# Kernel optimization log

Measured on AMD Instinct MI355X. Metric: run time of the kernel, lower is better.

## Reference

```python
import math
import jax, jax.numpy as jnp
from jax import lax
import numpy as np

SPARSITY = 0.05
EMBEDDING_SIZE = 2048
BATCH = 32768


def setup_inputs() -> dict:
    key = jax.random.key(0)
    k0, k1, k2 = jax.random.split(key, 3)
    x = jax.random.normal(k0, (BATCH, 28, 28), dtype=jnp.float32)
    # conv: out=5, in=1, k=3, no bias (kaiming-ish scale)
    conv_w = jax.random.normal(k1, (5, 1, 3, 3), dtype=jnp.float32) * (1.0 / math.sqrt(9))
    bn_gamma = jnp.ones((5,), jnp.float32)
    bn_beta = jnp.zeros((5,), jnp.float32)
    bn_mean = jnp.zeros((5,), jnp.float32)
    bn_var = jnp.ones((5,), jnp.float32)
    # fc: [EMBEDDING_SIZE, 320], no bias
    fc_w = jax.random.normal(k2, (EMBEDDING_SIZE, 5 * 8 * 8), dtype=jnp.float32) * (1.0 / math.sqrt(320))
    return {"x": x, "conv_w": conv_w, "bn_gamma": bn_gamma, "bn_beta": bn_beta,
            "bn_mean": bn_mean, "bn_var": bn_var, "fc_w": fc_w}


def _kwta(z):
    # k-winners-take-all: top k_active entries per row -> 1, rest -> 0.
    k_active = math.ceil(SPARSITY * z.shape[1])
    topv, _ = lax.top_k(z, k_active)          # [B, k]
    thr = topv[:, -1:]                         # kth largest per row
    binary = (z >= thr).astype(z.dtype)
    # straight-through: forward = binary, backward = identity
    return z + lax.stop_gradient(binary - z)


def reference(x, conv_w, bn_gamma, bn_beta, bn_mean, bn_var, fc_w):
    h = x[:, None, :, :]  # [B,1,28,28]
    h = lax.conv_general_dilated(h, conv_w, window_strides=(1, 1), padding="VALID",
                                 dimension_numbers=("NCHW", "OIHW", "NCHW"))  # [B,5,26,26]
    inv_std = bn_gamma / jnp.sqrt(bn_var + 1e-5)
    h = (h - bn_mean[None, :, None, None]) * inv_std[None, :, None, None] + bn_beta[None, :, None, None]
    h = jnp.maximum(h, 0.0)
    # max_pool2d(kernel=3, stride=3), floor mode -> [B,5,8,8]
    h = lax.reduce_window(h, -jnp.inf, lax.max, (1, 1, 3, 3), (1, 1, 3, 3), "VALID")
    h = h.reshape(h.shape[0], -1)              # [B,320]
    z = h @ fc_w.T                             # [B,EMBEDDING_SIZE]
    return _kwta(z)
```

## Files before the change

kernel.cpp:

```cpp
#include <hip/hip_runtime.h>
#include <math.h>

#define BATCH 32768
#define EMB   2048
#define KDIM  320
#define KACT  103

#define BM 16
#define GTHREADS 1024

#define CIMG 16

#define HSTRIDE 260

__global__ __launch_bounds__(256) void transpose_w_kernel(const float* __restrict__ W,
                                                          float* __restrict__ WT) {
  __shared__ float tile[32][33];
  const int k0 = blockIdx.x * 32;
  const int n0 = blockIdx.y * 32;
  const int tx = threadIdx.x;
  const int ty = threadIdx.y;
  for (int i = ty; i < 32; i += 8)
    tile[i][tx] = W[(size_t)(n0 + i) * KDIM + k0 + tx];
  __syncthreads();
  for (int i = ty; i < 32; i += 8)
    WT[(size_t)(k0 + i) * EMB + n0 + tx] = tile[tx][i];
}

__global__ __launch_bounds__(512) void conv_pool_kernel(const float* __restrict__ x,
                                                        const float* __restrict__ cw,
                                                        const float* __restrict__ gamma,
                                                        const float* __restrict__ beta,
                                                        const float* __restrict__ mean,
                                                        const float* __restrict__ var,
                                                        float* __restrict__ Ht) {
#pragma clang fp contract(off)
  __shared__ float xs[CIMG * 784];
  __shared__ float hs[KDIM * 17];
  __shared__ float wv[45];
  __shared__ float inv_s[5], mu_s[5], be_s[5];
  const int t  = threadIdx.x;
  const int b0 = blockIdx.x * CIMG;

  {
    const float4* src = (const float4*)(x + (size_t)b0 * 784);
    float4* dst = (float4*)xs;
    for (int i = t; i < CIMG * 196; i += 512) dst[i] = src[i];
  }
  if (t < 45) wv[t] = cw[t];
  if (t < 5) {
    inv_s[t] = gamma[t] / sqrtf(var[t] + 1e-5f);
    mu_s[t] = mean[t];
    be_s[t] = beta[t];
  }
  __syncthreads();

  const int i0   = t >> 6;
  const int lane = t & 63;
  const int py = lane >> 3;
  const int px = lane & 7;

  for (int ii = 0; ii < 2; ++ii) {
    const int img = i0 * 2 + ii;
    const float* xb = xs + img * 784;

    float xr[5][5];
#pragma unroll
    for (int i = 0; i < 5; ++i)
#pragma unroll
      for (int j = 0; j < 5; ++j)
        xr[i][j] = xb[(3 * py + i) * 28 + 3 * px + j];

#pragma unroll
    for (int c = 0; c < 5; ++c) {
      float wr[9];
#pragma unroll
      for (int i = 0; i < 9; ++i) wr[i] = wv[c * 9 + i];
      const float inv = inv_s[c], mu = mu_s[c], be = be_s[c];
      float mx = -__builtin_huge_valf();
#pragma unroll
      for (int ry = 0; ry < 3; ++ry)
#pragma unroll
        for (int rx = 0; rx < 3; ++rx) {
          float s = 0.0f;
#pragma unroll
          for (int di = 0; di < 3; ++di)
#pragma unroll
            for (int dj = 0; dj < 3; ++dj)
              s = __builtin_fmaf(xr[ry + di][rx + dj], wr[di * 3 + dj], s);
          float t1 = s - mu;
          float t2 = t1 * inv;
          float t3 = t2 + be;
          mx = fmaxf(mx, t3);
        }
      hs[(c * 64 + lane) * 17 + img] = fmaxf(mx, 0.0f);
    }
  }
  __syncthreads();

  float* dst = Ht + (size_t)blockIdx.x * (KDIM * CIMG);
  for (int i = t; i < KDIM * CIMG; i += 512) {
    const int k = i >> 4;
    const int img = i & 15;
    dst[i] = hs[k * 17 + img];
  }
}

__global__ __launch_bounds__(GTHREADS, 8) void gemm_topk_kernel(const float* __restrict__ Ht,
                                                                const float* __restrict__ WT,
                                                                float* __restrict__ out) {
  __shared__ unsigned histo[BM * HSTRIDE];
  __shared__ unsigned prefix_s[BM];
  __shared__ unsigned rank_s[BM];

  const int t    = threadIdx.x;
  const int lane = t & 63;
  const int w    = t >> 6;
  const int m0   = blockIdx.x * BM;
  const int nt   = t * 2;

  if (t < BM) { prefix_s[t] = 0u; rank_s[t] = KACT; }

  float acc[BM][2];
#pragma unroll
  for (int m = 0; m < BM; ++m) {
    acc[m][0] = 0.0f;
    acc[m][1] = 0.0f;
  }

  const float* Ap = Ht + (size_t)blockIdx.x * (KDIM * BM);
  const float* wp = WT + nt;

#pragma unroll 4
  for (int k = 0; k < KDIM; ++k) {
    const float* ak = Ap + (size_t)k * BM;
    float av[BM];
#pragma unroll
    for (int m = 0; m < BM; ++m) av[m] = ak[m];
    const float2 bb = *(const float2*)(wp + (size_t)k * EMB);
#pragma unroll
    for (int m = 0; m < BM; ++m) {
      acc[m][0] = __builtin_fmaf(av[m], bb.x, acc[m][0]);
      acc[m][1] = __builtin_fmaf(av[m], bb.y, acc[m][1]);
    }
  }
  __syncthreads();

  for (int pass = 0; pass < 4; ++pass) {
    const int shift = 24 - pass * 8;
    for (int i = t; i < BM * HSTRIDE; i += GTHREADS) histo[i] = 0u;
    unsigned pref[BM];
#pragma unroll
    for (int m = 0; m < BM; ++m) pref[m] = prefix_s[m];
    __syncthreads();
#pragma unroll
    for (int m = 0; m < BM; ++m) {
#pragma unroll
      for (int j = 0; j < 2; ++j) {
        unsigned u = __float_as_uint(acc[m][j]);
        u = (u & 0x80000000u) ? ~u : (u | 0x80000000u);
        const bool in = (pass == 0) || ((u >> (shift + 8)) == pref[m]);
        if (in) atomicAdd(&histo[m * HSTRIDE + ((u >> shift) & 255u)], 1u);
      }
    }
    __syncthreads();
    {
      const int m = w;
      const unsigned rank = rank_s[m];
      const uint4 c = *(const uint4*)(histo + m * HSTRIDE + lane * 4);
      const unsigned s = c.x + c.y + c.z + c.w;
      unsigned suf = s;
#pragma unroll
      for (int off = 1; off < 64; off <<= 1) {
        const unsigned o = __shfl_down(suf, off);
        if (lane + off < 64) suf += o;
      }
      const unsigned above = suf - s;
      if (above < rank && rank <= suf) {
        unsigned bin, newr;
        if (above + c.w >= rank)                    { bin = lane * 4 + 3; newr = rank - above; }
        else if (above + c.w + c.z >= rank)         { bin = lane * 4 + 2; newr = rank - above - c.w; }
        else if (above + c.w + c.z + c.y >= rank)   { bin = lane * 4 + 1; newr = rank - above - c.w - c.z; }
        else                                        { bin = lane * 4 + 0; newr = rank - above - c.w - c.z - c.y; }
        prefix_s[m] = (prefix_s[m] << 8) | bin;
        rank_s[m] = newr;
      }
    }
    __syncthreads();
  }

  unsigned thr[BM];
#pragma unroll
  for (int m = 0; m < BM; ++m) thr[m] = prefix_s[m];

#pragma unroll
  for (int m = 0; m < BM; ++m) {
    float2 o;
#pragma unroll
    for (int j = 0; j < 2; ++j) {
      unsigned u = __float_as_uint(acc[m][j]);
      u = (u & 0x80000000u) ? ~u : (u | 0x80000000u);
      ((float*)&o)[j] = (u >= thr[m]) ? 1.0f : 0.0f;
    }
    *(float2*)(out + (size_t)(m0 + m) * EMB + nt) = o;
  }
}

extern "C" void kernel_launch(void* const* d_in, const int* in_sizes, int n_in,
                              void* d_out, int out_size, void* d_ws, size_t ws_size,
                              hipStream_t stream) {
  const float* x      = (const float*)d_in[0];
  const float* conv_w = (const float*)d_in[1];
  const float* gamma  = (const float*)d_in[2];
  const float* beta   = (const float*)d_in[3];
  const float* mean   = (const float*)d_in[4];
  const float* var    = (const float*)d_in[5];
  const float* fc_w   = (const float*)d_in[6];
  float* out = (float*)d_out;

  float* Ht = (float*)d_ws;
  float* WT = (float*)d_ws + (size_t)KDIM * BATCH;

  transpose_w_kernel<<<dim3(KDIM / 32, EMB / 32), dim3(32, 8), 0, stream>>>(fc_w, WT);
  conv_pool_kernel<<<BATCH / CIMG, 512, 0, stream>>>(x, conv_w, gamma, beta, mean, var, Ht);
  gemm_topk_kernel<<<BATCH / BM, GTHREADS, 0, stream>>>(Ht, WT, out);
}
```

Before: 833.0 us.

## Replace shared-memory radix histogram top-k with per-wave ballot bitwise threshold search

Swaps the 4-pass 8-bit radix histogram selection, which relies on shared atomics, for a bit-by-bit binary search of the k-th largest key. Each wave loads one row of 2048 values from LDS into registers and counts candidates with ballot/popcount across 32 bit iterations. Rows are staged through an 8-row LDS buffer in two halves, so the block's 16 waves each take one row. This removes atomic contention and the histogram clears, but it adds 32 serial iterations of 32 ballots per wave and extra barriers.

```diff
diff --git a/kernel.cpp b/kernel.cpp
--- a/kernel.cpp
+++ b/kernel.cpp
@@ -10,8 +10,6 @@
 #define GTHREADS 1024
 
 #define CIMG 16
-
-#define HSTRIDE 260
 
 __global__ __launch_bounds__(256) void transpose_w_kernel(const float* __restrict__ W,
                                                           float* __restrict__ WT) {
@@ -109,9 +107,8 @@
 __global__ __launch_bounds__(GTHREADS, 8) void gemm_topk_kernel(const float* __restrict__ Ht,
                                                                 const float* __restrict__ WT,
                                                                 float* __restrict__ out) {
-  __shared__ unsigned histo[BM * HSTRIDE];
-  __shared__ unsigned prefix_s[BM];
-  __shared__ unsigned rank_s[BM];
+  __shared__ float zb[8][EMB];
+  __shared__ unsigned thr_s[BM];
 
   const int t    = threadIdx.x;
   const int lane = t & 63;
@@ -119,8 +116,6 @@
   const int m0   = blockIdx.x * BM;
   const int nt   = t * 2;
 
-  if (t < BM) { prefix_s[t] = 0u; rank_s[t] = KACT; }
-
   float acc[BM][2];
 #pragma unroll
   for (int m = 0; m < BM; ++m) {
@@ -144,64 +139,81 @@
       acc[m][1] = __builtin_fmaf(av[m], bb.y, acc[m][1]);
     }
   }
-  __syncthreads();
-
-  for (int pass = 0; pass < 4; ++pass) {
-    const int shift = 24 - pass * 8;
-    for (int i = t; i < BM * HSTRIDE; i += GTHREADS) histo[i] = 0u;
-    unsigned pref[BM];
-#pragma unroll
-    for (int m = 0; m < BM; ++m) pref[m] = prefix_s[m];
-    __syncthreads();
-#pragma unroll
-    for (int m = 0; m < BM; ++m) {
-#pragma unroll
-      for (int j = 0; j < 2; ++j) {
-        unsigned u = __float_as_uint(acc[m][j]);
-        u = (u & 0x80000000u) ? ~u : (u | 0x80000000u);
-        const bool in = (pass == 0) || ((u >> (shift + 8)) == pref[m]);
-        if (in) atomicAdd(&histo[m * HSTRIDE + ((u >> shift) & 255u)], 1u);
-      }
-    }
-    __syncthreads();
-    {
-      const int m = w;
-      const unsigned rank = rank_s[m];
-      const uint4 c = *(const uint4*)(histo + m * HSTRIDE + lane * 4);
-      const unsigned s = c.x + c.y + c.z + c.w;
-      unsigned suf = s;
-#pragma unroll
-      for (int off = 1; off < 64; off <<= 1) {
-        const unsigned o = __shfl_down(suf, off);
-        if (lane + off < 64) suf += o;
-      }
-      const unsigned above = suf - s;
-      if (above < rank && rank <= suf) {
-        unsigned bin, newr;
-        if (above + c.w >= rank)                    { bin = lane * 4 + 3; newr = rank - above; }
-        else if (above + c.w + c.z >= rank)         { bin = lane * 4 + 2; newr = rank - above - c.w; }
-        else if (above + c.w + c.z + c.y >= rank)   { bin = lane * 4 + 1; newr = rank - above - c.w - c.z; }
-        else                                        { bin = lane * 4 + 0; newr = rank - above - c.w - c.z - c.y; }
-        prefix_s[m] = (prefix_s[m] << 8) | bin;
-        rank_s[m] = newr;
-      }
-    }
-    __syncthreads();
-  }
-
-  unsigned thr[BM];
-#pragma unroll
-  for (int m = 0; m < BM; ++m) thr[m] = prefix_s[m];
-
-#pragma unroll
-  for (int m = 0; m < BM; ++m) {
+
+#pragma unroll
+  for (int m = 0; m < 8; ++m)
+    *(float2*)&zb[m][nt] = *(const float2*)&acc[8 + m][0];
+  __syncthreads();
+
+  if (w >= 8) {
+    const unsigned* row = (const unsigned*)&zb[w - 8][0];
+    unsigned v[32];
+#pragma unroll
+    for (int j = 0; j < 32; ++j) {
+      const unsigned x = row[j * 64 + lane];
+      v[j] = x ^ (unsigned)(((int)x >> 31) | 0x80000000);
+    }
+    unsigned T = 0u;
+    for (int b = 31; b >= 0; --b) {
+      const unsigned cand = T | (1u << b);
+      unsigned cnt = 0u;
+#pragma unroll
+      for (int j = 0; j < 32; ++j)
+        cnt += (unsigned)__popcll(__ballot(v[j] >= cand));
+      if (cnt >= KACT) T = cand;
+    }
+    if (lane == 0) thr_s[w] = T;
+  }
+  __syncthreads();
+
+#pragma unroll
+  for (int m = 0; m < 8; ++m) {
+    const float2 p = *(const float2*)&zb[m][nt];
+    const unsigned thr = thr_s[8 + m];
+    unsigned ux = __float_as_uint(p.x); ux ^= (unsigned)(((int)ux >> 31) | 0x80000000);
+    unsigned uy = __float_as_uint(p.y); uy ^= (unsigned)(((int)uy >> 31) | 0x80000000);
     float2 o;
-#pragma unroll
-    for (int j = 0; j < 2; ++j) {
-      unsigned u = __float_as_uint(acc[m][j]);
-      u = (u & 0x80000000u) ? ~u : (u | 0x80000000u);
-      ((float*)&o)[j] = (u >= thr[m]) ? 1.0f : 0.0f;
-    }
+    o.x = (ux >= thr) ? 1.0f : 0.0f;
+    o.y = (uy >= thr) ? 1.0f : 0.0f;
+    *(float2*)(out + (size_t)(m0 + 8 + m) * EMB + nt) = o;
+  }
+  __syncthreads();
+
+#pragma unroll
+  for (int m = 0; m < 8; ++m)
+    *(float2*)&zb[m][nt] = *(const float2*)&acc[m][0];
+  __syncthreads();
+
+  if (w < 8) {
+    const unsigned* row = (const unsigned*)&zb[w][0];
+    unsigned v[32];
+#pragma unroll
+    for (int j = 0; j < 32; ++j) {
+      const unsigned x = row[j * 64 + lane];
+      v[j] = x ^ (unsigned)(((int)x >> 31) | 0x80000000);
+    }
+    unsigned T = 0u;
+    for (int b = 31; b >= 0; --b) {
+      const unsigned cand = T | (1u << b);
+      unsigned cnt = 0u;
+#pragma unroll
+      for (int j = 0; j < 32; ++j)
+        cnt += (unsigned)__popcll(__ballot(v[j] >= cand));
+      if (cnt >= KACT) T = cand;
+    }
+    if (lane == 0) thr_s[w] = T;
+  }
+  __syncthreads();
+
+#pragma unroll
+  for (int m = 0; m < 8; ++m) {
+    const float2 p = *(const float2*)&zb[m][nt];
+    const unsigned thr = thr_s[m];
+    unsigned ux = __float_as_uint(p.x); ux ^= (unsigned)(((int)ux >> 31) | 0x80000000);
+    unsigned uy = __float_as_uint(p.y); uy ^= (unsigned)(((int)uy >> 31) | 0x80000000);
+    float2 o;
+    o.x = (ux >= thr) ? 1.0f : 0.0f;
+    o.y = (uy >= thr) ? 1.0f : 0.0f;
     *(float2*)(out + (size_t)(m0 + m) * EMB + nt) = o;
   }
 }
```

Result: slower. 884.8 us (+6.2%).

## Fuse conv/pool stage into the GEMM+top-k kernel in one launch

Applied to the files above, without the earlier changes.

Merges the conv+BN+ReLU+pool kernel into the GEMM/top-k kernel, so each 1024-thread block computes features for its 16 images and then does the GEMM and radix-select top-k. Shared memory is aliased so the input tile, feature buffer and histogram share one array. Features are still written to global memory and read back through a separate pointer, relying on block-local visibility after __syncthreads. This removes one launch and lets conv work overlap other blocks' GEMM, at the cost of larger shared memory per block and possibly lower occupancy.

```diff
diff --git a/kernel.cpp b/kernel.cpp
--- a/kernel.cpp
+++ b/kernel.cpp
@@ -8,7 +8,6 @@
 
 #define BM 16
 #define GTHREADS 1024
-
 #define CIMG 16
 
 #define HSTRIDE 260
@@ -27,25 +26,37 @@
     WT[(size_t)(k0 + i) * EMB + n0 + tx] = tile[tx][i];
 }
 
-__global__ __launch_bounds__(512) void conv_pool_kernel(const float* __restrict__ x,
-                                                        const float* __restrict__ cw,
-                                                        const float* __restrict__ gamma,
-                                                        const float* __restrict__ beta,
-                                                        const float* __restrict__ mean,
-                                                        const float* __restrict__ var,
-                                                        float* __restrict__ Ht) {
+__global__ __launch_bounds__(GTHREADS, 8) void fused_conv_gemm_topk(
+    const float* __restrict__ x,
+    const float* __restrict__ cw,
+    const float* __restrict__ gamma,
+    const float* __restrict__ beta,
+    const float* __restrict__ mean,
+    const float* __restrict__ var,
+    float* __restrict__ HtW,
+    const float* __restrict__ HtR,
+    const float* __restrict__ WT,
+    float* __restrict__ out) {
 #pragma clang fp contract(off)
-  __shared__ float xs[CIMG * 784];
-  __shared__ float hs[KDIM * 17];
+  __shared__ __attribute__((aligned(16))) float smem[17984];
   __shared__ float wv[45];
   __shared__ float inv_s[5], mu_s[5], be_s[5];
-  const int t  = threadIdx.x;
-  const int b0 = blockIdx.x * CIMG;
+  __shared__ unsigned prefix_s[BM];
+  __shared__ unsigned rank_s[BM];
+
+  float* const xs = smem;
+  float* const hs = smem + 12544;
+  unsigned* const histo = (unsigned*)smem;
+
+  const int t    = threadIdx.x;
+  const int lane = t & 63;
+  const int w    = t >> 6;
+  const int b0   = blockIdx.x * CIMG;
 
   {
     const float4* src = (const float4*)(x + (size_t)b0 * 784);
     float4* dst = (float4*)xs;
-    for (int i = t; i < CIMG * 196; i += 512) dst[i] = src[i];
+    for (int i = t; i < CIMG * 196; i += GTHREADS) dst[i] = src[i];
   }
   if (t < 45) wv[t] = cw[t];
   if (t < 5) {
@@ -55,14 +66,11 @@
   }
   __syncthreads();
 
-  const int i0   = t >> 6;
-  const int lane = t & 63;
-  const int py = lane >> 3;
-  const int px = lane & 7;
-
-  for (int ii = 0; ii < 2; ++ii) {
-    const int img = i0 * 2 + ii;
+  {
+    const int img = w;
     const float* xb = xs + img * 784;
+    const int py = lane >> 3;
+    const int px = lane & 7;
 
     float xr[5][5];
 #pragma unroll
@@ -98,28 +106,19 @@
   }
   __syncthreads();
 
-  float* dst = Ht + (size_t)blockIdx.x * (KDIM * CIMG);
-  for (int i = t; i < KDIM * CIMG; i += 512) {
-    const int k = i >> 4;
-    const int img = i & 15;
-    dst[i] = hs[k * 17 + img];
-  }
-}
-
-__global__ __launch_bounds__(GTHREADS, 8) void gemm_topk_kernel(const float* __restrict__ Ht,
-                                                                const float* __restrict__ WT,
-                                                                float* __restrict__ out) {
-  __shared__ unsigned histo[BM * HSTRIDE];
-  __shared__ unsigned prefix_s[BM];
-  __shared__ unsigned rank_s[BM];
-
-  const int t    = threadIdx.x;
-  const int lane = t & 63;
-  const int w    = t >> 6;
-  const int m0   = blockIdx.x * BM;
-  const int nt   = t * 2;
-
+  {
+    float* dst = HtW + (size_t)blockIdx.x * (KDIM * CIMG);
+    for (int i = t; i < KDIM * CIMG; i += GTHREADS) {
+      const int k = i >> 4;
+      const int img = i & 15;
+      dst[i] = hs[k * 17 + img];
+    }
+  }
   if (t < BM) { prefix_s[t] = 0u; rank_s[t] = KACT; }
+  __syncthreads();
+
+  const int m0 = blockIdx.x * BM;
+  const int nt = t * 2;
 
   float acc[BM][2];
 #pragma unroll
@@ -128,7 +127,7 @@
     acc[m][1] = 0.0f;
   }
 
-  const float* Ap = Ht + (size_t)blockIdx.x * (KDIM * BM);
+  const float* Ap = HtR + (size_t)blockIdx.x * (KDIM * BM);
   const float* wp = WT + nt;
 
 #pragma unroll 4
@@ -222,6 +221,6 @@
   float* WT = (float*)d_ws + (size_t)KDIM * BATCH;
 
   transpose_w_kernel<<<dim3(KDIM / 32, EMB / 32), dim3(32, 8), 0, stream>>>(fc_w, WT);
-  conv_pool_kernel<<<BATCH / CIMG, 512, 0, stream>>>(x, conv_w, gamma, beta, mean, var, Ht);
-  gemm_topk_kernel<<<BATCH / BM, GTHREADS, 0, stream>>>(Ht, WT, out);
+  fused_conv_gemm_topk<<<BATCH / CIMG, GTHREADS, 0, stream>>>(
+      x, conv_w, gamma, beta, mean, var, Ht, Ht, WT, out);
 }
```

After: 804.7 us. -3.4%, faster.
